# Performance work log

Hardware: AMD Instinct MI355X
Metric: run time of the kernel (lower is better)

## Reference

```python
import jax, jax.numpy as jnp
import numpy as np

N_NODES = 10000
N_EDGES = 160000
ATOMIC_DIM = 16          # C: multiplicity of 0e input irreps
L_VALUES = [0, 1, 2]
EDGE_DIM = 16            # number of bessel basis functions
HIDDEN_DIM = 16          # H: multiplicity of each output irrep
RADIUS_CUTOFF = 6.0
DEGREE_NORM = 16.0
SILU_GAIN = 1.679177     # e3nn normalize2mom gain for silu
WEIGHT_NUMEL = len(L_VALUES) * ATOMIC_DIM * HIDDEN_DIM  # 768


def bessel_basis(dist, num_basis, cutoff):
    # e3nn soft_one_hot_linspace, basis='bessel', start=0, cutoff=True
    x = dist[:, None]                                   # [E,1]
    n = jnp.arange(1, num_basis + 1, dtype=dist.dtype) * jnp.pi
    x_safe = jnp.where(x > 0, x, 1.0)
    out = jnp.sqrt(2.0 / cutoff) * jnp.sin(n * x / cutoff) / x_safe
    out = out * ((x < cutoff) & (x > 0))
    return out * jnp.sqrt(float(num_basis))             # EdgeEmbedding scaling


def spherical_harmonics(u):
    # e3nn real spherical harmonics l=0,1,2, 'component' convention, then
    # 'integral' normalization (divide by sqrt(4*pi)). u: unit vectors [E,3].
    x, y, z = u[:, 0], u[:, 1], u[:, 2]
    s3, s5, s15 = jnp.sqrt(3.0), jnp.sqrt(5.0), jnp.sqrt(15.0)
    y0 = jnp.ones_like(x)[:, None]
    y1 = jnp.stack([s3 * x, s3 * y, s3 * z], axis=-1)
    y2 = jnp.stack([
        s15 * x * z,
        s15 * x * y,
        s5 * (y * y - 0.5 * (x * x + z * z)),
        s15 * y * z,
        0.5 * s15 * (z * z - x * x),
    ], axis=-1)
    Y = jnp.concatenate([y0, y1, y2], axis=-1)          # [E, 9]
    return Y / jnp.sqrt(4.0 * jnp.pi)


def setup_inputs() -> dict:
    key = jax.random.key(0)
    k1, k2, k3, k4, k5 = jax.random.split(key, 5)
    atomic_features = jax.random.normal(k1, (N_NODES, ATOMIC_DIM), dtype=jnp.float32)
    coords = jax.random.normal(k2, (N_NODES, 3), dtype=jnp.float32) * 3.0
    edge_index = jax.random.randint(k3, (2, N_EDGES), 0, N_NODES, dtype=jnp.int64)
    W1 = jax.random.normal(k4, (EDGE_DIM, HIDDEN_DIM), dtype=jnp.float32)
    W2 = jax.random.normal(k5, (HIDDEN_DIM, WEIGHT_NUMEL), dtype=jnp.float32)
    return {"atomic_features": atomic_features, "coords": coords,
            "edge_index": edge_index, "W1": W1, "W2": W2}


def reference(atomic_features, coords, edge_index, W1, W2):
    src, dst = edge_index[0], edge_index[1]
    rel = coords[src] - coords[dst]                     # [E,3]
    dist = jnp.linalg.norm(rel, axis=-1)                # [E]
    # 1. spherical harmonic projection of normalized edge vectors
    u = rel / jnp.maximum(dist, 1e-12)[:, None]
    Y = spherical_harmonics(u)                          # [E,9]
    # 2. radial bessel basis
    eb = bessel_basis(dist, EDGE_DIM, RADIUS_CUTOFF)    # [E,edge_dim]
    # 3. FC net (e3nn FullyConnectedNet: /sqrt(fan_in), normalized silu)
    h = SILU_GAIN * jax.nn.silu(eb @ W1 / jnp.sqrt(float(EDGE_DIM)))
    edge_z = h @ W2 / jnp.sqrt(float(HIDDEN_DIM))       # [E, weight_numel]
    # 4. fully-connected tensor product Cx0e x (1x0e+1x1o+1x2e) -> Hx(...)
    E = edge_z.shape[0]
    w = edge_z.reshape(E, len(L_VALUES), ATOMIC_DIM, HIDDEN_DIM)
    xs = atomic_features[src]                           # [E,C]
    inv_sqrt_c = 1.0 / jnp.sqrt(float(ATOMIC_DIM))      # e3nn path normalization
    outs, off = [], 0
    for i, l in enumerate(L_VALUES):
        d = 2 * l + 1
        Yl = Y[:, off:off + d]                          # [E,d]
        m = jnp.einsum('ec,em,ech->ehm', xs, Yl, w[:, i]) * inv_sqrt_c
        outs.append(m.reshape(E, HIDDEN_DIM * d))
        off += d
    messages = jnp.concatenate(outs, axis=-1)           # [E, H*9]
    # 5. scatter-aggregate by destination node, degree normalization
    hidden = jax.ops.segment_sum(messages, dst, num_segments=N_NODES)
    return hidden / DEGREE_NORM
```

## Files before the change

kernel.cpp:

```cpp
#include <hip/hip_runtime.h>
#include <hip/hip_bf16.h>
#include <math.h>


typedef __attribute__((ext_vector_type(8))) short short8;
typedef __attribute__((ext_vector_type(4))) float f32x4;
typedef __attribute__((ext_vector_type(4))) unsigned short u16x4;

#define DSTRIDE 72

static __device__ __forceinline__ unsigned short f2bf(float f) {
  __hip_bfloat16 h = __float2bfloat16(f);
  return __builtin_bit_cast(unsigned short, h);
}
static __device__ __forceinline__ float bf2f(unsigned short s) {
  unsigned u = ((unsigned)s) << 16;
  return __builtin_bit_cast(float, u);
}

__global__ __launch_bounds__(256)
void prep_kernel(const float* __restrict__ W2, unsigned short* __restrict__ w2f,
                 int* __restrict__ head, int N) {
  int gid = blockIdx.x * 256 + threadIdx.x;
  if (gid < N) head[gid] = -1;
  if (gid < 24 * 64) {
    int fi = gid >> 6, lane = gid & 63;
    int s = fi / 3, t = fi - 3 * s;
    int h = lane & 15, kq = lane >> 4;
    short8 pack;
    #pragma unroll
    for (int j = 0; j < 8; ++j) {
      int kg = s * 32 + kq * 8 + j;
      int kk = kg >> 4, c = kg & 15;
      pack[j] = (short)f2bf(W2[kk * 768 + t * 256 + c * 16 + h]);
    }
    *(short8*)&w2f[(size_t)gid * 8] = pack;
  }
}

__global__ __launch_bounds__(256, 3)
void interact_kernel(const float* __restrict__ xfeat,
                     const float* __restrict__ coords,
                     const int* __restrict__ eidx,
                     const float* __restrict__ W1g,
                     const unsigned short* __restrict__ w2f,
                     unsigned short* __restrict__ data,
                     int* __restrict__ head,
                     int* __restrict__ next,
                     int E)
{
  __shared__ __align__(16) float W1s[256];
  __shared__ float hsS[256 * 20];
  __shared__ __align__(16) unsigned short xsS[256 * 24];
  __shared__ int eS[256];
  __shared__ int wsum[4];

  const int tid  = threadIdx.x;
  const int lane = tid & 63, wid = tid >> 6;
  W1s[tid] = W1g[tid];

  const int e = blockIdx.x * 256 + tid;
  bool act = false;
  int src = 0, dst = 0;
  float rx = 0.f, ry = 0.f, rz = 0.f, d2 = 0.f;
  if (e < E) {
    src = eidx[e]; dst = eidx[E + e];
    rx = coords[3*src]   - coords[3*dst];
    ry = coords[3*src+1] - coords[3*dst+1];
    rz = coords[3*src+2] - coords[3*dst+2];
    d2 = rx*rx + ry*ry + rz*rz;
    act = (d2 > 0.0f) && (d2 < 36.0f);
  }
  const float4 xv0 = *(const float4*)&xfeat[src*16 + 0];
  const float4 xv1 = *(const float4*)&xfeat[src*16 + 4];
  const float4 xv2 = *(const float4*)&xfeat[src*16 + 8];
  const float4 xv3 = *(const float4*)&xfeat[src*16 + 12];

  unsigned long long bm = __ballot(act);
  int pfx = __popcll(bm & ((1ull << lane) - 1ull));
  if (lane == 0) wsum[wid] = __popcll(bm);
  __syncthreads();
  int base = 0;
  #pragma unroll
  for (int w = 0; w < 4; ++w) base += (w < wid) ? wsum[w] : 0;
  const int total = wsum[0] + wsum[1] + wsum[2] + wsum[3];
  const int cpos = base + pfx;

  if (act) {
    float dd  = sqrtf(d2);
    float inv = 1.0f / dd;
    float x = rx*inv, y = ry*inv, z = rz*inv;
    const float A1 = 0.48860251190291992f;
    const float A2 = 1.09254843059207907f;
    const float A3 = 0.63078313050504001f;
    unsigned short* dr = data + (size_t)e * DSTRIDE;
    short8 ys;
    ys[0] = (short)f2bf(A1*x);   ys[1] = (short)f2bf(A1*y);  ys[2] = (short)f2bf(A1*z);
    ys[3] = (short)f2bf(A2*x*z); ys[4] = (short)f2bf(A2*x*y);
    ys[5] = (short)f2bf(A3*(y*y - 0.5f*(x*x + z*z)));
    ys[6] = (short)f2bf(A2*y*z); ys[7] = (short)f2bf(0.5f*A2*(z*z - x*x));
    *(short8*)&dr[64] = ys;
    next[e] = atomicExch(&head[dst], e);

    float theta = 0.52359877559829887f * dd;
    float s1 = __sinf(theta), c1 = __cosf(theta);
    float snm = 0.0f, sn = s1;
    float4 hbv[4];
    #pragma unroll
    for (int q = 0; q < 4; ++q) hbv[q] = make_float4(0.f, 0.f, 0.f, 0.f);
    #pragma unroll
    for (int k = 0; k < 16; ++k) {
      #pragma unroll
      for (int q = 0; q < 4; ++q) {
        const float4 w = *((const float4*)&W1s[k*16 + q*4]);
        hbv[q].x = fmaf(sn, w.x, hbv[q].x);
        hbv[q].y = fmaf(sn, w.y, hbv[q].y);
        hbv[q].z = fmaf(sn, w.z, hbv[q].z);
        hbv[q].w = fmaf(sn, w.w, hbv[q].w);
      }
      float sp = 2.0f*c1*sn - snm;
      snm = sn; sn = sp;
    }
    const float scale1 = 2.30940107675850305f * inv * 0.25f;
    float* hrow = &hsS[cpos * 20];
    #pragma unroll
    for (int q = 0; q < 4; ++q) {
      float b[4] = {hbv[q].x, hbv[q].y, hbv[q].z, hbv[q].w};
      #pragma unroll
      for (int r = 0; r < 4; ++r) {
        float p = b[r] * scale1;
        hrow[q*4 + r] = 1.679177f * p / (1.0f + __expf(-p));
      }
    }
    unsigned short* xrow = &xsS[cpos * 24];
    xrow[ 0] = f2bf(xv0.x); xrow[ 1] = f2bf(xv0.y); xrow[ 2] = f2bf(xv0.z); xrow[ 3] = f2bf(xv0.w);
    xrow[ 4] = f2bf(xv1.x); xrow[ 5] = f2bf(xv1.y); xrow[ 6] = f2bf(xv1.z); xrow[ 7] = f2bf(xv1.w);
    xrow[ 8] = f2bf(xv2.x); xrow[ 9] = f2bf(xv2.y); xrow[10] = f2bf(xv2.z); xrow[11] = f2bf(xv2.w);
    xrow[12] = f2bf(xv3.x); xrow[13] = f2bf(xv3.y); xrow[14] = f2bf(xv3.z); xrow[15] = f2bf(xv3.w);
    eS[cpos] = e;
  }
  const int padded = (total + 15) & ~15;
  if (tid >= total && tid < padded) {
    #pragma unroll
    for (int j = 0; j < 16; ++j) hsS[tid*20 + j] = 0.0f;
    #pragma unroll
    for (int j = 0; j < 16; ++j) xsS[tid*24 + j] = 0;
  }
  __syncthreads();

  short8 bfr[8][3];
  #pragma unroll
  for (int s = 0; s < 8; ++s)
    #pragma unroll
    for (int t = 0; t < 3; ++t)
      bfr[s][t] = *(const short8*)&w2f[(size_t)((s*3 + t)*64 + lane) * 8];

  const int ngroups = padded >> 4;
  const int ma = lane & 15, kq = lane >> 4;
  const int c0 = (kq & 1) * 8;
  for (int g = wid; g < ngroups; g += 4) {
    const int cidx = g*16 + ma;
    const float* hrow = &hsS[cidx * 20];
    const unsigned short* xrow = &xsS[cidx * 24];
    float xsf[8];
    #pragma unroll
    for (int j = 0; j < 8; ++j) xsf[j] = bf2f(xrow[c0 + j]);

    f32x4 acc0 = {0,0,0,0}, acc1 = {0,0,0,0}, acc2 = {0,0,0,0};
    #pragma unroll
    for (int s = 0; s < 8; ++s) {
      const float hk = hrow[2*s + (kq >> 1)];
      short8 a;
      #pragma unroll
      for (int j = 0; j < 8; ++j) a[j] = (short)f2bf(hk * xsf[j]);
      acc0 = __builtin_amdgcn_mfma_f32_16x16x32_bf16(a, bfr[s][0], acc0, 0, 0, 0);
      acc1 = __builtin_amdgcn_mfma_f32_16x16x32_bf16(a, bfr[s][1], acc1, 0, 0, 0);
      acc2 = __builtin_amdgcn_mfma_f32_16x16x32_bf16(a, bfr[s][2], acc2, 0, 0, 0);
    }
    const float sc = 0.00390625f;
    #pragma unroll
    for (int r = 0; r < 4; ++r) {
      const int cr = g*16 + kq*4 + r;
      if (cr < total) {
        unsigned short* dr = data + (size_t)eS[cr] * DSTRIDE;
        u16x4 vv;
        vv[0] = f2bf(acc0[r] * sc);
        vv[1] = f2bf(acc1[r] * sc);
        vv[2] = f2bf(acc2[r] * sc);
        vv[3] = 0;
        *(u16x4*)&dr[ma * 4] = vv;
      }
    }
  }
}

__global__ __launch_bounds__(256)
void gather_kernel(const unsigned short* __restrict__ data,
                   const int* __restrict__ head,
                   const int* __restrict__ next,
                   float* __restrict__ out, int N)
{
  int gid = blockIdx.x * 256 + threadIdx.x;
  int node = gid >> 4, h = gid & 15;
  if (node >= N) return;

  float a0 = 0.f;
  float a10 = 0.f, a11 = 0.f, a12 = 0.f;
  float a20 = 0.f, a21 = 0.f, a22 = 0.f, a23 = 0.f, a24 = 0.f;

  int p = head[node];
  while (p >= 0) {
    const unsigned short* dr = data + (size_t)p * DSTRIDE;
    int pn = next[p];
    u16x4 vv = *(const u16x4*)&dr[h * 4];
    short8 yv = *(const short8*)&dr[64];
    float v0 = bf2f(vv[0]), v1 = bf2f(vv[1]), v2 = bf2f(vv[2]);
    a0  += v0;
    a10 = fmaf(v1, bf2f((unsigned short)yv[0]), a10);
    a11 = fmaf(v1, bf2f((unsigned short)yv[1]), a11);
    a12 = fmaf(v1, bf2f((unsigned short)yv[2]), a12);
    a20 = fmaf(v2, bf2f((unsigned short)yv[3]), a20);
    a21 = fmaf(v2, bf2f((unsigned short)yv[4]), a21);
    a22 = fmaf(v2, bf2f((unsigned short)yv[5]), a22);
    a23 = fmaf(v2, bf2f((unsigned short)yv[6]), a23);
    a24 = fmaf(v2, bf2f((unsigned short)yv[7]), a24);
    p = pn;
  }

  float* o = out + (size_t)node * 144;
  o[h] = a0 * 0.28209479177387814f;
  o[16 + h*3 + 0] = a10;
  o[16 + h*3 + 1] = a11;
  o[16 + h*3 + 2] = a12;
  o[64 + h*5 + 0] = a20;
  o[64 + h*5 + 1] = a21;
  o[64 + h*5 + 2] = a22;
  o[64 + h*5 + 3] = a23;
  o[64 + h*5 + 4] = a24;
}

extern "C" void kernel_launch(void* const* d_in, const int* in_sizes, int n_in,
                              void* d_out, int out_size, void* d_ws, size_t ws_size,
                              hipStream_t stream) {
  const float* xfeat  = (const float*)d_in[0];
  const float* coords = (const float*)d_in[1];
  const int*   eidx   = (const int*)d_in[2];
  const float* W1     = (const float*)d_in[3];
  const float* W2     = (const float*)d_in[4];
  float* out = (float*)d_out;

  const int E = in_sizes[2] / 2;
  const int N = out_size / 144;

  char* ws = (char*)d_ws;
  size_t off_head = (size_t)E * DSTRIDE * sizeof(unsigned short);
  size_t off_next = off_head + (size_t)((N + 3) & ~3) * sizeof(int);
  size_t off_w2f  = off_next + (size_t)E * sizeof(int);
  unsigned short* data = (unsigned short*)ws;
  int* head = (int*)(ws + off_head);
  int* next = (int*)(ws + off_next);
  unsigned short* w2f = (unsigned short*)(ws + off_w2f);

  int pblk = (N + 255) / 256;
  if (pblk < 6) pblk = 6;
  prep_kernel<<<pblk, 256, 0, stream>>>(W2, w2f, head, N);
  interact_kernel<<<(E + 255) / 256, 256, 0, stream>>>(xfeat, coords, eidx, W1,
                                                       w2f, data, head, next, E);
  gather_kernel<<<(N * 16 + 255) / 256, 256, 0, stream>>>(data, head, next, out, N);
}
```

Baseline: 38.06 us.

## Split each edge across four threads and stream W2 fragments from memory

Each block now handles 64 edges instead of 256, with four lanes per edge. Each lane computes a quarter of the hidden radial features and a quarter of the source features, and shared buffers shrink to match. The W2 fragments are no longer preloaded into registers; each MFMA step reloads them from global/L2, and the launch bound now allows higher occupancy. The goal is more parallelism in the per-edge scalar work and less register and LDS pressure. The cost is redundant distance and trig work per lane, four times as many blocks, and repeated W2 loads inside the MFMA loop.

```diff
diff --git a/kernel.cpp b/kernel.cpp
--- a/kernel.cpp
+++ b/kernel.cpp
@@ -38,7 +38,7 @@
   }
 }
 
-__global__ __launch_bounds__(256, 3)
+__global__ __launch_bounds__(256, 4)
 void interact_kernel(const float* __restrict__ xfeat,
                      const float* __restrict__ coords,
                      const int* __restrict__ eidx,
@@ -50,16 +50,18 @@
                      int E)
 {
   __shared__ __align__(16) float W1s[256];
-  __shared__ float hsS[256 * 20];
-  __shared__ __align__(16) unsigned short xsS[256 * 24];
-  __shared__ int eS[256];
+  __shared__ float hsS[64 * 20];
+  __shared__ __align__(16) unsigned short xsS[64 * 24];
+  __shared__ int eS[64];
   __shared__ int wsum[4];
 
   const int tid  = threadIdx.x;
   const int lane = tid & 63, wid = tid >> 6;
+  const int q    = lane & 3;
+  const int el   = wid * 16 + (lane >> 2);
   W1s[tid] = W1g[tid];
 
-  const int e = blockIdx.x * 256 + tid;
+  const int e = blockIdx.x * 64 + el;
   bool act = false;
   int src = 0, dst = 0;
   float rx = 0.f, ry = 0.f, rz = 0.f, d2 = 0.f;
@@ -71,14 +73,12 @@
     d2 = rx*rx + ry*ry + rz*rz;
     act = (d2 > 0.0f) && (d2 < 36.0f);
   }
-  const float4 xv0 = *(const float4*)&xfeat[src*16 + 0];
-  const float4 xv1 = *(const float4*)&xfeat[src*16 + 4];
-  const float4 xv2 = *(const float4*)&xfeat[src*16 + 8];
-  const float4 xv3 = *(const float4*)&xfeat[src*16 + 12];
+  const float4 xq = *(const float4*)&xfeat[src*16 + q*4];
 
   unsigned long long bm = __ballot(act);
-  int pfx = __popcll(bm & ((1ull << lane) - 1ull));
-  if (lane == 0) wsum[wid] = __popcll(bm);
+  unsigned long long emask = bm & 0x1111111111111111ull;
+  int pfx = __popcll(emask & ((1ull << (4 * (lane >> 2))) - 1ull));
+  if (lane == 0) wsum[wid] = __popcll(emask);
   __syncthreads();
   int base = 0;
   #pragma unroll
@@ -89,71 +89,58 @@
   if (act) {
     float dd  = sqrtf(d2);
     float inv = 1.0f / dd;
-    float x = rx*inv, y = ry*inv, z = rz*inv;
-    const float A1 = 0.48860251190291992f;
-    const float A2 = 1.09254843059207907f;
-    const float A3 = 0.63078313050504001f;
-    unsigned short* dr = data + (size_t)e * DSTRIDE;
-    short8 ys;
-    ys[0] = (short)f2bf(A1*x);   ys[1] = (short)f2bf(A1*y);  ys[2] = (short)f2bf(A1*z);
-    ys[3] = (short)f2bf(A2*x*z); ys[4] = (short)f2bf(A2*x*y);
-    ys[5] = (short)f2bf(A3*(y*y - 0.5f*(x*x + z*z)));
-    ys[6] = (short)f2bf(A2*y*z); ys[7] = (short)f2bf(0.5f*A2*(z*z - x*x));
-    *(short8*)&dr[64] = ys;
-    next[e] = atomicExch(&head[dst], e);
-
+    if (q == 0) {
+      float x = rx*inv, y = ry*inv, z = rz*inv;
+      const float A1 = 0.48860251190291992f;
+      const float A2 = 1.09254843059207907f;
+      const float A3 = 0.63078313050504001f;
+      unsigned short* dr = data + (size_t)e * DSTRIDE;
+      short8 ys;
+      ys[0] = (short)f2bf(A1*x);   ys[1] = (short)f2bf(A1*y);  ys[2] = (short)f2bf(A1*z);
+      ys[3] = (short)f2bf(A2*x*z); ys[4] = (short)f2bf(A2*x*y);
+      ys[5] = (short)f2bf(A3*(y*y - 0.5f*(x*x + z*z)));
+      ys[6] = (short)f2bf(A2*y*z); ys[7] = (short)f2bf(0.5f*A2*(z*z - x*x));
+      *(short8*)&dr[64] = ys;
+      next[e] = atomicExch(&head[dst], e);
+      eS[cpos] = e;
+    }
     float theta = 0.52359877559829887f * dd;
     float s1 = __sinf(theta), c1 = __cosf(theta);
     float snm = 0.0f, sn = s1;
-    float4 hbv[4];
-    #pragma unroll
-    for (int q = 0; q < 4; ++q) hbv[q] = make_float4(0.f, 0.f, 0.f, 0.f);
+    float4 hb = make_float4(0.f, 0.f, 0.f, 0.f);
     #pragma unroll
     for (int k = 0; k < 16; ++k) {
-      #pragma unroll
-      for (int q = 0; q < 4; ++q) {
-        const float4 w = *((const float4*)&W1s[k*16 + q*4]);
-        hbv[q].x = fmaf(sn, w.x, hbv[q].x);
-        hbv[q].y = fmaf(sn, w.y, hbv[q].y);
-        hbv[q].z = fmaf(sn, w.z, hbv[q].z);
-        hbv[q].w = fmaf(sn, w.w, hbv[q].w);
-      }
+      const float4 w = *((const float4*)&W1s[k*16 + q*4]);
+      hb.x = fmaf(sn, w.x, hb.x);
+      hb.y = fmaf(sn, w.y, hb.y);
+      hb.z = fmaf(sn, w.z, hb.z);
+      hb.w = fmaf(sn, w.w, hb.w);
       float sp = 2.0f*c1*sn - snm;
       snm = sn; sn = sp;
     }
     const float scale1 = 2.30940107675850305f * inv * 0.25f;
-    float* hrow = &hsS[cpos * 20];
-    #pragma unroll
-    for (int q = 0; q < 4; ++q) {
-      float b[4] = {hbv[q].x, hbv[q].y, hbv[q].z, hbv[q].w};
+    float4 hv;
+    {
+      float b[4] = {hb.x, hb.y, hb.z, hb.w};
+      float* op = (float*)&hv;
       #pragma unroll
       for (int r = 0; r < 4; ++r) {
         float p = b[r] * scale1;
-        hrow[q*4 + r] = 1.679177f * p / (1.0f + __expf(-p));
+        op[r] = 1.679177f * p / (1.0f + __expf(-p));
       }
     }
-    unsigned short* xrow = &xsS[cpos * 24];
-    xrow[ 0] = f2bf(xv0.x); xrow[ 1] = f2bf(xv0.y); xrow[ 2] = f2bf(xv0.z); xrow[ 3] = f2bf(xv0.w);
-    xrow[ 4] = f2bf(xv1.x); xrow[ 5] = f2bf(xv1.y); xrow[ 6] = f2bf(xv1.z); xrow[ 7] = f2bf(xv1.w);
-    xrow[ 8] = f2bf(xv2.x); xrow[ 9] = f2bf(xv2.y); xrow[10] = f2bf(xv2.z); xrow[11] = f2bf(xv2.w);
-    xrow[12] = f2bf(xv3.x); xrow[13] = f2bf(xv3.y); xrow[14] = f2bf(xv3.z); xrow[15] = f2bf(xv3.w);
-    eS[cpos] = e;
+    *(float4*)&hsS[cpos * 20 + q * 4] = hv;
+    u16x4 xp;
+    xp[0] = f2bf(xq.x); xp[1] = f2bf(xq.y); xp[2] = f2bf(xq.z); xp[3] = f2bf(xq.w);
+    *(u16x4*)&xsS[cpos * 24 + q * 4] = xp;
   }
   const int padded = (total + 15) & ~15;
-  if (tid >= total && tid < padded) {
-    #pragma unroll
-    for (int j = 0; j < 16; ++j) hsS[tid*20 + j] = 0.0f;
-    #pragma unroll
-    for (int j = 0; j < 16; ++j) xsS[tid*24 + j] = 0;
+  if (el >= total && el < padded) {
+    *(float4*)&hsS[el * 20 + q * 4] = make_float4(0.f, 0.f, 0.f, 0.f);
+    u16x4 z; z[0] = 0; z[1] = 0; z[2] = 0; z[3] = 0;
+    *(u16x4*)&xsS[el * 24 + q * 4] = z;
   }
   __syncthreads();
-
-  short8 bfr[8][3];
-  #pragma unroll
-  for (int s = 0; s < 8; ++s)
-    #pragma unroll
-    for (int t = 0; t < 3; ++t)
-      bfr[s][t] = *(const short8*)&w2f[(size_t)((s*3 + t)*64 + lane) * 8];
 
   const int ngroups = padded >> 4;
   const int ma = lane & 15, kq = lane >> 4;
@@ -173,9 +160,12 @@
       short8 a;
       #pragma unroll
       for (int j = 0; j < 8; ++j) a[j] = (short)f2bf(hk * xsf[j]);
-      acc0 = __builtin_amdgcn_mfma_f32_16x16x32_bf16(a, bfr[s][0], acc0, 0, 0, 0);
-      acc1 = __builtin_amdgcn_mfma_f32_16x16x32_bf16(a, bfr[s][1], acc1, 0, 0, 0);
-      acc2 = __builtin_amdgcn_mfma_f32_16x16x32_bf16(a, bfr[s][2], acc2, 0, 0, 0);
+      const short8 b0 = *(const short8*)&w2f[(size_t)((s*3 + 0)*64 + lane) * 8];
+      const short8 b1 = *(const short8*)&w2f[(size_t)((s*3 + 1)*64 + lane) * 8];
+      const short8 b2 = *(const short8*)&w2f[(size_t)((s*3 + 2)*64 + lane) * 8];
+      acc0 = __builtin_amdgcn_mfma_f32_16x16x32_bf16(a, b0, acc0, 0, 0, 0);
+      acc1 = __builtin_amdgcn_mfma_f32_16x16x32_bf16(a, b1, acc1, 0, 0, 0);
+      acc2 = __builtin_amdgcn_mfma_f32_16x16x32_bf16(a, b2, acc2, 0, 0, 0);
     }
     const float sc = 0.00390625f;
     #pragma unroll
@@ -264,7 +254,7 @@
   int pblk = (N + 255) / 256;
   if (pblk < 6) pblk = 6;
   prep_kernel<<<pblk, 256, 0, stream>>>(W2, w2f, head, N);
-  interact_kernel<<<(E + 255) / 256, 256, 0, stream>>>(xfeat, coords, eidx, W1,
-                                                       w2f, data, head, next, E);
+  interact_kernel<<<(E + 63) / 64, 256, 0, stream>>>(xfeat, coords, eidx, W1,
+                                                     w2f, data, head, next, E);
   gather_kernel<<<(N * 16 + 255) / 256, 256, 0, stream>>>(data, head, next, out, N);
 }
```

After: 41.58 us. 1.09x slower.
